# Optimization experiments

Hardware: AMD Instinct MI355X
Metric: run time of the kernel (lower is better)

## Reference

```python
import jax, jax.numpy as jnp
import numpy as np

COEFS = [1.5, 1.2, 1.0, 0.9, 0.82, 0.69, 0.65, 0.56]  # self.coefs reversed
COMMITMENT_COST = 0.4


def number_to_pair(n):
    if n == 1:
        return (0, 1)
    m = (n - 1) // 2
    e = 1 if (n % 2 == 0) else 0
    return (2 * m + 3 + e - 1, 2 * m + 4 + e - 1)


def build_codebooks(weight, num_levels):
    # Level-l codebook has 2^l vectors, built as sums of pairs of rows of `weight`.
    d = weight.shape[1]
    cbs = []
    prev = None
    for stage in range(1, num_levels + 1):
        i0, i1 = number_to_pair(stage)
        vecs = weight[i0:i1 + 1]            # [2, d]
        if stage == 1:
            cb = vecs
        else:
            cb = (prev[:, None, :] + vecs[None, :, :]).reshape(-1, d)
        cbs.append(cb)
        prev = cb
    return cbs


def quantize(cb, flat):
    dists = (jnp.sum(flat ** 2, axis=1, keepdims=True)
             + jnp.sum(cb ** 2, axis=1)
             - 2.0 * flat @ cb.T)           # [N, K]
    idx = jnp.argmin(dists, axis=1)          # [N]
    return jnp.take(cb, idx, axis=0)         # == one-hot @ cb


def setup_inputs() -> dict:
    key = jax.random.key(0)
    k1, k2 = jax.random.split(key)
    B, d, H, W = 16, 128, 64, 64
    p = 256
    inputs = jax.random.normal(k1, (B, d, H, W), dtype=jnp.float32)
    weight = jax.random.normal(k2, (p, d), dtype=jnp.float32)  # nn.Embedding default N(0,1)
    return {"inputs": inputs, "weight": weight, "num_vectors": 256}


def reference(inputs, weight, num_vectors):
    num_levels = int(np.log2(num_vectors))   # 8
    x = jnp.transpose(inputs, (0, 2, 3, 1))  # [B, H, W, d]
    d = x.shape[-1]
    flat = x.reshape(-1, d)                  # [N, d]
    cbs = build_codebooks(weight, num_levels)

    quant_vecs = []
    losses = []
    for level in range(num_levels):
        q = quantize(cbs[level], flat).reshape(x.shape)
        e_latent = jnp.mean((jax.lax.stop_gradient(q) - x) ** 2)
        q_latent = jnp.mean((jax.lax.stop_gradient(x) - q) ** 2)
        losses.append(COEFS[level] * q_latent + COMMITMENT_COST * e_latent)
        st = x + jax.lax.stop_gradient(q - x)             # straight-through
        quant_vecs.append(jnp.transpose(st, (0, 3, 1, 2)))  # back to [B, d, H, W]

    return jnp.stack(quant_vecs), jnp.stack(losses)
```

## Files before the change

kernel.cpp:

```cpp
#include <hip/hip_runtime.h>

typedef unsigned long long u64;

#define OFF_A      0
#define OFF_DT     512
#define OFF_V0T    1536
#define OFF_BASET  2560
#define OFF_IDX_BYTES 16384
#define OFF_PART_F    135168

__device__ __forceinline__ float warp_sum(float v) {
  #pragma unroll
  for (int off = 32; off > 0; off >>= 1) v += __shfl_down(v, off);
  return v;
}

__global__ __launch_bounds__(64) void build_tables(const float* __restrict__ w,
                                                   float* __restrict__ wsf) {
  const int r0[8] = {0, 3, 4, 5, 6, 7, 8, 9};
  int e = blockIdx.x;
  int t = threadIdx.x;
  if (e < 510) {
    int ep2 = e + 2;
    int L = 31 - __clz(ep2);
    int i = ep2 - (1 << L);
    float acc = 0.f;
    #pragma unroll
    for (int half = 0; half < 2; ++half) {
      int cc = t + half * 64;
      float v = 0.f;
      for (int s = 0; s < L; ++s) {
        int b = (i >> (L - 1 - s)) & 1;
        v += w[(r0[s] + b) * 128 + cc];
      }
      acc += v * v;
    }
    acc = warp_sum(acc);
    if (t == 0) wsf[OFF_A + e] = -0.5f * acc;
  } else {
    #pragma unroll
    for (int half = 0; half < 2; ++half) {
      int cc = t + half * 64;
      float basesum = 0.f;
      #pragma unroll
      for (int s = 0; s < 8; ++s) {
        float w0 = w[r0[s] * 128 + cc];
        float w1 = w[(r0[s] + 1) * 128 + cc];
        wsf[OFF_V0T + cc * 8 + s] = w0;
        wsf[OFF_DT + cc * 8 + s] = w1 - w0;
        basesum += w0;
        wsf[OFF_BASET + s * 128 + cc] = basesum;
      }
    }
  }
}

template <int L, int I, int N>
struct SU {
  static __device__ __forceinline__ void run(const float* Al, const float* T,
                                             const float* S, float& bs, int& bi) {
    float dot;
    if constexpr (L <= 4) {
      dot = T[I << (4 - L)];
    } else {
      dot = T[I >> (L - 4)] + S[(I & ((1 << (L - 4)) - 1)) << (8 - L)];
    }
    float sc = dot + Al[I];
    if (sc > bs) { bs = sc; bi = I; }
    SU<L, I + 1, N>::run(Al, T, S, bs, bi);
  }
};
template <int L, int N>
struct SU<L, N, N> {
  static __device__ __forceinline__ void run(const float*, const float*, const float*,
                                             float&, int&) {}
};

template <int L>
__device__ __forceinline__ void search_level(const float* Al_base, const float* T,
                                             const float* S, float& bestsc, int& bestidx) {
  const float* Al = Al_base + ((1 << L) - 2);
  float bs = -3.4e38f;
  int bi = 0;
  SU<L, 0, (1 << L)>::run(Al, T, S, bs, bi);
  bestsc = bs;
  bestidx = bi;
}

__global__ __launch_bounds__(256) void search_kernel(const float* __restrict__ in,
                                                     const float* __restrict__ tbl,
                                                     float* __restrict__ partial,
                                                     u64* __restrict__ idxp) {
  __shared__ float dTl[1024];
  __shared__ float v0l[1024];
  __shared__ float Al[512];
  __shared__ float part[256][17];
  __shared__ float lsc[4][64];
  __shared__ int   lix[4][64];

  int tid = threadIdx.x;
  for (int i = tid; i < 1024; i += 256) { dTl[i] = tbl[OFF_DT + i]; v0l[i] = tbl[OFF_V0T + i]; }
  if (tid < 255) { Al[tid] = tbl[OFF_A + tid]; Al[tid + 255] = tbl[OFF_A + tid + 255]; }
  __syncthreads();

  int q = tid >> 6;
  int posl = tid & 63;
  int gpos = blockIdx.x * 64 + posl;
  int b = gpos >> 12;
  int hw = gpos & 4095;
  const float* xp = in + ((size_t)b << 19) + ((size_t)(q * 32) << 12) + hw;

  float qq[8], uu[8];
  #pragma unroll
  for (int k = 0; k < 8; ++k) { qq[k] = 0.f; uu[k] = 0.f; }
  float xx = 0.f;
  int cbase = q * 32;
  float xv[16];
  #pragma unroll
  for (int g = 0; g < 2; ++g) {
    #pragma unroll
    for (int j = 0; j < 16; ++j) xv[j] = xp[(size_t)(g * 16 + j) << 12];
    #pragma unroll
    for (int j = 0; j < 16; ++j) {
      float x = xv[j];
      int c = cbase + g * 16 + j;
      xx = fmaf(x, x, xx);
      #pragma unroll
      for (int k = 0; k < 8; ++k) {
        qq[k] = fmaf(x, dTl[c * 8 + k], qq[k]);
        uu[k] = fmaf(x, v0l[c * 8 + k], uu[k]);
      }
    }
  }

  #pragma unroll
  for (int k = 0; k < 8; ++k) { part[tid][k] = qq[k]; part[tid][8 + k] = uu[k]; }
  part[tid][16] = xx;
  __syncthreads();
  #pragma unroll
  for (int p = 1; p < 4; ++p) {
    int ptn = tid ^ (p << 6);
    #pragma unroll
    for (int k = 0; k < 8; ++k) { qq[k] += part[ptn][k]; uu[k] += part[ptn][8 + k]; }
    xx += part[ptn][16];
  }

  float T[16], S[16];
  #pragma unroll
  for (int h = 0; h < 16; ++h) {
    float tv = 0.f, sv = 0.f;
    if (h & 8) { tv += qq[0]; sv += qq[4]; }
    if (h & 4) { tv += qq[1]; sv += qq[5]; }
    if (h & 2) { tv += qq[2]; sv += qq[6]; }
    if (h & 1) { tv += qq[3]; sv += qq[7]; }
    T[h] = tv; S[h] = sv;
  }

  float bsc[4];
  int bix[4];
  if (q == 3) {
    float bs; int bi;
    search_level<8>(Al, T, S, bs, bi);
    lsc[3][posl] = bs; lix[3][posl] = bi;
  } else if (q == 2) {
    float bs; int bi;
    search_level<7>(Al, T, S, bs, bi);
    lsc[2][posl] = bs; lix[2][posl] = bi;
  } else if (q == 1) {
    float bs; int bi;
    search_level<5>(Al, T, S, bs, bi);
    lsc[0][posl] = bs; lix[0][posl] = bi;
    search_level<6>(Al, T, S, bs, bi);
    lsc[1][posl] = bs; lix[1][posl] = bi;
  } else {
    search_level<1>(Al, T, S, bsc[0], bix[0]);
    search_level<2>(Al, T, S, bsc[1], bix[1]);
    search_level<3>(Al, T, S, bsc[2], bix[2]);
    search_level<4>(Al, T, S, bsc[3], bix[3]);
  }
  __syncthreads();

  if (q == 0) {
    float s5 = lsc[0][posl], s6 = lsc[1][posl], s7 = lsc[2][posl], s8 = lsc[3][posl];
    int i5 = lix[0][posl], i6 = lix[1][posl], i7 = lix[2][posl], i8 = lix[3][posl];
    u64 pk = (u64)bix[0] | ((u64)bix[1] << 1) | ((u64)bix[2] << 3) | ((u64)bix[3] << 6) |
             ((u64)i5 << 10) | ((u64)i6 << 15) | ((u64)i7 << 21) | ((u64)i8 << 28);
    idxp[gpos] = pk;
    float ball[8] = {bsc[0], bsc[1], bsc[2], bsc[3], s5, s6, s7, s8};
    float P0 = 0.f;
    #pragma unroll
    for (int l = 0; l < 8; ++l) {
      P0 += uu[l];
      float sse = xx - 2.f * (P0 + ball[l]);
      sse = warp_sum(sse);
      if (tid == 0) partial[l * 1024 + blockIdx.x] = sse;
    }
  }
}

template <int LV>
__device__ __forceinline__ void write_level(const float* dTl, const float* btl,
                                            const u64* __restrict__ idxp, int pos,
                                            float4* __restrict__ op) {
  constexpr int SHv = (LV == 1 ? 0 : LV == 2 ? 1 : LV == 3 ? 3 : LV == 4 ? 6 :
                       LV == 5 ? 10 : LV == 6 ? 15 : LV == 7 ? 21 : 28);
  float bf[4][LV];
  #pragma unroll
  for (int p = 0; p < 4; ++p) {
    u64 pk = idxp[pos + p];
    int idx = (int)((pk >> SHv) & ((1u << LV) - 1));
    #pragma unroll
    for (int s = 0; s < LV; ++s) bf[p][s] = (float)((idx >> (LV - 1 - s)) & 1);
  }
  #pragma unroll 2
  for (int c = 0; c < 128; ++c) {
    float bt = btl[c];
    float dv[LV];
    #pragma unroll
    for (int s = 0; s < LV; ++s) dv[s] = dTl[c * 8 + s];
    float q0 = bt, q1 = bt, q2 = bt, q3 = bt;
    #pragma unroll
    for (int s = 0; s < LV; ++s) {
      q0 = fmaf(bf[0][s], dv[s], q0);
      q1 = fmaf(bf[1][s], dv[s], q1);
      q2 = fmaf(bf[2][s], dv[s], q2);
      q3 = fmaf(bf[3][s], dv[s], q3);
    }
    float4 r; r.x = q0; r.y = q1; r.z = q2; r.w = q3;
    op[(size_t)c << 10] = r;
  }
}

__global__ __launch_bounds__(256) void write_kernel(const float* __restrict__ tbl,
                                                    const u64* __restrict__ idxp,
                                                    float* __restrict__ out) {
  __shared__ float dTl[1024];
  __shared__ float btl[128];
  int blk = blockIdx.x;
  int L = blk >> 6;
  for (int i = threadIdx.x; i < 1024; i += 256) dTl[i] = tbl[OFF_DT + i];
  if (threadIdx.x < 128) btl[threadIdx.x] = tbl[OFF_BASET + L * 128 + threadIdx.x];
  __syncthreads();

  if (blk == 0 && threadIdx.x < 64) {
    const float CO[8] = {1.5f, 1.2f, 1.0f, 0.9f, 0.82f, 0.69f, 0.65f, 0.56f};
    const float* partial = tbl + OFF_PART_F;
    int t = threadIdx.x;
    int l = t >> 3;
    int j = t & 7;
    float s = 0.f;
    #pragma unroll 4
    for (int k = 0; k < 128; ++k) s += partial[l * 1024 + j + k * 8];
    s += __shfl_down(s, 4);
    s += __shfl_down(s, 2);
    s += __shfl_down(s, 1);
    if (j == 0)
      out[67108864ull + l] = (CO[l] + 0.4f) * s * (1.0f / 8388608.0f);
  }

  int g = (blk & 63) * 256 + threadIdx.x;
  int pos = g << 2;
  int bb = pos >> 12;
  int hw = pos & 4095;
  float4* op = (float4*)(out + (((size_t)(L * 16 + bb)) << 19) + hw);
  switch (L) {
    case 0: write_level<1>(dTl, btl, idxp, pos, op); break;
    case 1: write_level<2>(dTl, btl, idxp, pos, op); break;
    case 2: write_level<3>(dTl, btl, idxp, pos, op); break;
    case 3: write_level<4>(dTl, btl, idxp, pos, op); break;
    case 4: write_level<5>(dTl, btl, idxp, pos, op); break;
    case 5: write_level<6>(dTl, btl, idxp, pos, op); break;
    case 6: write_level<7>(dTl, btl, idxp, pos, op); break;
    case 7: write_level<8>(dTl, btl, idxp, pos, op); break;
  }
}

extern "C" void kernel_launch(void* const* d_in, const int* in_sizes, int n_in,
                              void* d_out, int out_size, void* d_ws, size_t ws_size,
                              hipStream_t stream) {
  const float* in = (const float*)d_in[0];
  const float* w  = (const float*)d_in[1];
  float* wsf = (float*)d_ws;
  u64* idxp = (u64*)((char*)d_ws + OFF_IDX_BYTES);
  float* partial = wsf + OFF_PART_F;
  float* out = (float*)d_out;

  build_tables<<<511, 64, 0, stream>>>(w, wsf);
  search_kernel<<<1024, 256, 0, stream>>>(in, wsf, partial, idxp);
  write_kernel<<<512, 256, 0, stream>>>(wsf, idxp, out);
}
```

Measured before the change: 352.2 us.

## Give each search thread a full pixel and use nontemporal loads/stores

```diff
diff --git a/kernel.cpp b/kernel.cpp
--- a/kernel.cpp
+++ b/kernel.cpp
@@ -1,6 +1,7 @@
 #include <hip/hip_runtime.h>
 
 typedef unsigned long long u64;
+typedef float nfloat4 __attribute__((ext_vector_type(4)));
 
 #define OFF_A      0
 #define OFF_DT     512
@@ -91,58 +92,49 @@
                                                      const float* __restrict__ tbl,
                                                      float* __restrict__ partial,
                                                      u64* __restrict__ idxp) {
-  __shared__ float dTl[1024];
-  __shared__ float v0l[1024];
+  __shared__ __align__(16) float dTl[1024];
+  __shared__ __align__(16) float v0l[1024];
   __shared__ float Al[512];
-  __shared__ float part[256][17];
-  __shared__ float lsc[4][64];
-  __shared__ int   lix[4][64];
+  __shared__ float red[4][8];
 
   int tid = threadIdx.x;
   for (int i = tid; i < 1024; i += 256) { dTl[i] = tbl[OFF_DT + i]; v0l[i] = tbl[OFF_V0T + i]; }
   if (tid < 255) { Al[tid] = tbl[OFF_A + tid]; Al[tid + 255] = tbl[OFF_A + tid + 255]; }
   __syncthreads();
 
-  int q = tid >> 6;
-  int posl = tid & 63;
-  int gpos = blockIdx.x * 64 + posl;
-  int b = gpos >> 12;
-  int hw = gpos & 4095;
-  const float* xp = in + ((size_t)b << 19) + ((size_t)(q * 32) << 12) + hw;
+  int pos = blockIdx.x * 256 + tid;
+  int b = pos >> 12;
+  int hw = pos & 4095;
+  const float* xp = in + ((size_t)b << 19) + hw;
+  const float4* dT4 = (const float4*)dTl;
+  const float4* v04 = (const float4*)v0l;
 
   float qq[8], uu[8];
   #pragma unroll
   for (int k = 0; k < 8; ++k) { qq[k] = 0.f; uu[k] = 0.f; }
   float xx = 0.f;
-  int cbase = q * 32;
-  float xv[16];
-  #pragma unroll
-  for (int g = 0; g < 2; ++g) {
-    #pragma unroll
-    for (int j = 0; j < 16; ++j) xv[j] = xp[(size_t)(g * 16 + j) << 12];
-    #pragma unroll
-    for (int j = 0; j < 16; ++j) {
+  #pragma unroll
+  for (int g = 0; g < 4; ++g) {
+    float xv[32];
+    #pragma unroll
+    for (int j = 0; j < 32; ++j)
+      xv[j] = __builtin_nontemporal_load(&xp[(size_t)(g * 32 + j) << 12]);
+    #pragma unroll
+    for (int j = 0; j < 32; ++j) {
       float x = xv[j];
-      int c = cbase + g * 16 + j;
+      int c = g * 32 + j;
+      float4 d0 = dT4[2 * c], d1 = dT4[2 * c + 1];
+      float4 u0 = v04[2 * c], u1 = v04[2 * c + 1];
       xx = fmaf(x, x, xx);
-      #pragma unroll
-      for (int k = 0; k < 8; ++k) {
-        qq[k] = fmaf(x, dTl[c * 8 + k], qq[k]);
-        uu[k] = fmaf(x, v0l[c * 8 + k], uu[k]);
-      }
-    }
-  }
-
-  #pragma unroll
-  for (int k = 0; k < 8; ++k) { part[tid][k] = qq[k]; part[tid][8 + k] = uu[k]; }
-  part[tid][16] = xx;
-  __syncthreads();
-  #pragma unroll
-  for (int p = 1; p < 4; ++p) {
-    int ptn = tid ^ (p << 6);
-    #pragma unroll
-    for (int k = 0; k < 8; ++k) { qq[k] += part[ptn][k]; uu[k] += part[ptn][8 + k]; }
-    xx += part[ptn][16];
+      qq[0] = fmaf(x, d0.x, qq[0]); qq[1] = fmaf(x, d0.y, qq[1]);
+      qq[2] = fmaf(x, d0.z, qq[2]); qq[3] = fmaf(x, d0.w, qq[3]);
+      qq[4] = fmaf(x, d1.x, qq[4]); qq[5] = fmaf(x, d1.y, qq[5]);
+      qq[6] = fmaf(x, d1.z, qq[6]); qq[7] = fmaf(x, d1.w, qq[7]);
+      uu[0] = fmaf(x, u0.x, uu[0]); uu[1] = fmaf(x, u0.y, uu[1]);
+      uu[2] = fmaf(x, u0.z, uu[2]); uu[3] = fmaf(x, u0.w, uu[3]);
+      uu[4] = fmaf(x, u1.x, uu[4]); uu[5] = fmaf(x, u1.y, uu[5]);
+      uu[6] = fmaf(x, u1.z, uu[6]); uu[7] = fmaf(x, u1.w, uu[7]);
+    }
   }
 
   float T[16], S[16];
@@ -156,52 +148,40 @@
     T[h] = tv; S[h] = sv;
   }
 
-  float bsc[4];
-  int bix[4];
-  if (q == 3) {
-    float bs; int bi;
-    search_level<8>(Al, T, S, bs, bi);
-    lsc[3][posl] = bs; lix[3][posl] = bi;
-  } else if (q == 2) {
-    float bs; int bi;
-    search_level<7>(Al, T, S, bs, bi);
-    lsc[2][posl] = bs; lix[2][posl] = bi;
-  } else if (q == 1) {
-    float bs; int bi;
-    search_level<5>(Al, T, S, bs, bi);
-    lsc[0][posl] = bs; lix[0][posl] = bi;
-    search_level<6>(Al, T, S, bs, bi);
-    lsc[1][posl] = bs; lix[1][posl] = bi;
-  } else {
-    search_level<1>(Al, T, S, bsc[0], bix[0]);
-    search_level<2>(Al, T, S, bsc[1], bix[1]);
-    search_level<3>(Al, T, S, bsc[2], bix[2]);
-    search_level<4>(Al, T, S, bsc[3], bix[3]);
+  float bsc[8];
+  int bix[8];
+  search_level<1>(Al, T, S, bsc[0], bix[0]);
+  search_level<2>(Al, T, S, bsc[1], bix[1]);
+  search_level<3>(Al, T, S, bsc[2], bix[2]);
+  search_level<4>(Al, T, S, bsc[3], bix[3]);
+  search_level<5>(Al, T, S, bsc[4], bix[4]);
+  search_level<6>(Al, T, S, bsc[5], bix[5]);
+  search_level<7>(Al, T, S, bsc[6], bix[6]);
+  search_level<8>(Al, T, S, bsc[7], bix[7]);
+
+  u64 pk = (u64)bix[0] | ((u64)bix[1] << 1) | ((u64)bix[2] << 3) | ((u64)bix[3] << 6) |
+           ((u64)bix[4] << 10) | ((u64)bix[5] << 15) | ((u64)bix[6] << 21) |
+           ((u64)bix[7] << 28);
+  idxp[pos] = pk;
+
+  int wv = tid >> 6;
+  float P0 = 0.f;
+  #pragma unroll
+  for (int l = 0; l < 8; ++l) {
+    P0 += uu[l];
+    float sse = xx - 2.f * (P0 + bsc[l]);
+    sse = warp_sum(sse);
+    if ((tid & 63) == 0) red[wv][l] = sse;
   }
   __syncthreads();
-
-  if (q == 0) {
-    float s5 = lsc[0][posl], s6 = lsc[1][posl], s7 = lsc[2][posl], s8 = lsc[3][posl];
-    int i5 = lix[0][posl], i6 = lix[1][posl], i7 = lix[2][posl], i8 = lix[3][posl];
-    u64 pk = (u64)bix[0] | ((u64)bix[1] << 1) | ((u64)bix[2] << 3) | ((u64)bix[3] << 6) |
-             ((u64)i5 << 10) | ((u64)i6 << 15) | ((u64)i7 << 21) | ((u64)i8 << 28);
-    idxp[gpos] = pk;
-    float ball[8] = {bsc[0], bsc[1], bsc[2], bsc[3], s5, s6, s7, s8};
-    float P0 = 0.f;
-    #pragma unroll
-    for (int l = 0; l < 8; ++l) {
-      P0 += uu[l];
-      float sse = xx - 2.f * (P0 + ball[l]);
-      sse = warp_sum(sse);
-      if (tid == 0) partial[l * 1024 + blockIdx.x] = sse;
-    }
-  }
+  if (tid < 8)
+    partial[tid * 256 + blockIdx.x] = red[0][tid] + red[1][tid] + red[2][tid] + red[3][tid];
 }
 
 template <int LV>
 __device__ __forceinline__ void write_level(const float* dTl, const float* btl,
                                             const u64* __restrict__ idxp, int pos,
-                                            float4* __restrict__ op) {
+                                            nfloat4* __restrict__ op) {
   constexpr int SHv = (LV == 1 ? 0 : LV == 2 ? 1 : LV == 3 ? 3 : LV == 4 ? 6 :
                        LV == 5 ? 10 : LV == 6 ? 15 : LV == 7 ? 21 : 28);
   float bf[4][LV];
@@ -226,8 +206,8 @@
       q2 = fmaf(bf[2][s], dv[s], q2);
       q3 = fmaf(bf[3][s], dv[s], q3);
     }
-    float4 r; r.x = q0; r.y = q1; r.z = q2; r.w = q3;
-    op[(size_t)c << 10] = r;
+    nfloat4 r = {q0, q1, q2, q3};
+    __builtin_nontemporal_store(r, &op[(size_t)c << 10]);
   }
 }
 
@@ -250,7 +230,7 @@
     int j = t & 7;
     float s = 0.f;
     #pragma unroll 4
-    for (int k = 0; k < 128; ++k) s += partial[l * 1024 + j + k * 8];
+    for (int k = 0; k < 32; ++k) s += partial[l * 256 + j + k * 8];
     s += __shfl_down(s, 4);
     s += __shfl_down(s, 2);
     s += __shfl_down(s, 1);
@@ -262,7 +242,7 @@
   int pos = g << 2;
   int bb = pos >> 12;
   int hw = pos & 4095;
-  float4* op = (float4*)(out + (((size_t)(L * 16 + bb)) << 19) + hw);
+  nfloat4* op = (nfloat4*)(out + (((size_t)(L * 16 + bb)) << 19) + hw);
   switch (L) {
     case 0: write_level<1>(dTl, btl, idxp, pos, op); break;
     case 1: write_level<2>(dTl, btl, idxp, pos, op); break;
@@ -286,6 +266,6 @@
   float* out = (float*)d_out;
 
   build_tables<<<511, 64, 0, stream>>>(w, wsf);
-  search_kernel<<<1024, 256, 0, stream>>>(in, wsf, partial, idxp);
+  search_kernel<<<256, 256, 0, stream>>>(in, wsf, partial, idxp);
   write_kernel<<<512, 256, 0, stream>>>(wsf, idxp, out);
 }
```

After: 789.4 us. +124.2%, slower.
